# Kernel optimization log

Measured on AMD Instinct MI355X. Metric: run time of the kernel, lower is better.

## Reference

```python
import jax, jax.numpy as jnp
import numpy as np

C_Z = 128
C_HIDDEN = 32
N_HEAD = 4
HC = N_HEAD * C_HIDDEN  # 128
LN_EPS = 1e-5


def setup_inputs() -> dict:
    key = jax.random.key(0)
    ks = jax.random.split(key, 8)
    b, n = 1, 256
    s = 1.0 / np.sqrt(C_Z)
    return {
        "z_ij": jax.random.normal(ks[0], (b, n, n, C_Z), dtype=jnp.float32),
        "ln_gamma": jnp.ones((C_Z,), dtype=jnp.float32),
        "ln_beta": jnp.zeros((C_Z,), dtype=jnp.float32),
        "Wq": jax.random.normal(ks[1], (C_Z, HC), dtype=jnp.float32) * s,
        "Wk": jax.random.normal(ks[2], (C_Z, HC), dtype=jnp.float32) * s,
        "Wv": jax.random.normal(ks[3], (C_Z, HC), dtype=jnp.float32) * s,
        "Wb": jax.random.normal(ks[4], (C_Z, N_HEAD), dtype=jnp.float32) * s,
        "Wg": jax.random.normal(ks[5], (C_Z, HC), dtype=jnp.float32) * s,
        "Wout": jax.random.normal(ks[6], (HC, C_Z), dtype=jnp.float32) * (1.0 / np.sqrt(HC)),
    }


def reference(z_ij, ln_gamma, ln_beta, Wq, Wk, Wv, Wb, Wg, Wout):
    b, n, _, _ = z_ij.shape
    # LayerNorm over c_z
    mu = jnp.mean(z_ij, axis=-1, keepdims=True)
    var = jnp.var(z_ij, axis=-1, keepdims=True)
    z = (z_ij - mu) * jax.lax.rsqrt(var + LN_EPS) * ln_gamma + ln_beta

    def heads(x):  # [b,i,j,hc] -> [b,i,j,h,d]
        return x.reshape(b, n, n, N_HEAD, C_HIDDEN)

    q = heads(z @ Wq)
    k = heads(z @ Wk)
    v = heads(z @ Wv)
    bias = z @ Wb                      # [b,i,j,h]
    g = jax.nn.sigmoid(heads(z @ Wg))  # [b,i,j,h,d]

    scores = jnp.einsum('bijhd,bikhd->bijkh', q, k) / np.sqrt(C_HIDDEN)
    scores = scores + bias[:, None]    # bias[b, j, k, h] broadcast over i
    a = jax.nn.softmax(scores, axis=-2)  # over k
    o = jnp.einsum('bijkh,bikhd->bijhd', a, v)
    o = (g * o).reshape(b, n, n, HC)
    return o @ Wout
```

## Files before the change

### kernel.cpp

```cpp
#include <hip/hip_runtime.h>

typedef _Float16 f16x8 __attribute__((ext_vector_type(8)));
typedef _Float16 f16x2 __attribute__((ext_vector_type(2)));
typedef float f32x4 __attribute__((ext_vector_type(4)));

#define MFMA16(a, b, c) __builtin_amdgcn_mfma_f32_16x16x32_f16(a, b, c, 0, 0, 0)

#define NROW 65536
#define SEGB 16777216ull

__global__ __launch_bounds__(256) void k_ln(
    const float* __restrict__ z, const float* __restrict__ gamma,
    const float* __restrict__ beta, const float* __restrict__ Wb,
    const float* __restrict__ Wq, const float* __restrict__ Wk,
    const float* __restrict__ Wv, const float* __restrict__ Wg,
    const float* __restrict__ Wout,
    _Float16* __restrict__ zln, float* __restrict__ biasT,
    _Float16* __restrict__ WtAll)
{
  __shared__ _Float16 sw[32 * 136];
  int bid = blockIdx.x;
  if (bid < 16384) {
    int lane = threadIdx.x & 63;
    int w = threadIdx.x >> 6;
    int row = bid * 4 + w;
    float2 v = ((const float2*)(z + (size_t)row * 128))[lane];
    float s = v.x + v.y;
    #pragma unroll
    for (int m = 1; m < 64; m <<= 1) s += __shfl_xor(s, m);
    float mu = s * 0.0078125f;
    float dx = v.x - mu, dy = v.y - mu;
    float q = dx * dx + dy * dy;
    #pragma unroll
    for (int m = 1; m < 64; m <<= 1) q += __shfl_xor(q, m);
    float rs = rsqrtf(q * 0.0078125f + 1e-5f);
    float2 g2 = ((const float2*)gamma)[lane];
    float2 b2 = ((const float2*)beta)[lane];
    float y0 = dx * rs * g2.x + b2.x;
    float y1 = dy * rs * g2.y + b2.y;
    f16x2 pr; pr.x = (_Float16)y0; pr.y = (_Float16)y1;
    *(f16x2*)(zln + (size_t)row * 128 + 2 * lane) = pr;
    float4 wb0 = ((const float4*)Wb)[2 * lane];
    float4 wb1 = ((const float4*)Wb)[2 * lane + 1];
    float pb0 = y0 * wb0.x + y1 * wb1.x;
    float pb1 = y0 * wb0.y + y1 * wb1.y;
    float pb2 = y0 * wb0.z + y1 * wb1.z;
    float pb3 = y0 * wb0.w + y1 * wb1.w;
    #pragma unroll
    for (int m = 1; m < 64; m <<= 1) {
      pb0 += __shfl_xor(pb0, m);
      pb1 += __shfl_xor(pb1, m);
      pb2 += __shfl_xor(pb2, m);
      pb3 += __shfl_xor(pb3, m);
    }
    if (lane == 0) {
      biasT[row] = pb0;
      biasT[NROW + row] = pb1;
      biasT[2 * NROW + row] = pb2;
      biasT[3 * NROW + row] = pb3;
    }
  } else {
    int t = bid - 16384;
    int mat = t >> 2, n0 = (t & 3) * 32;
    const float* src = (mat == 0) ? Wq : (mat == 1) ? Wk : (mat == 2) ? Wv
                       : (mat == 3) ? Wg : Wout;
    _Float16* dst = WtAll + mat * 16384;
    for (int it = 0; it < 16; ++it) {
      int e = threadIdx.x + it * 256;
      int c = e >> 5, j = e & 31;
      sw[j * 136 + c] = (_Float16)src[c * 128 + n0 + j];
    }
    __syncthreads();
    for (int it = 0; it < 2; ++it) {
      int ch = threadIdx.x + it * 256;
      int n = ch >> 4, k8 = (ch & 15) * 8;
      *(int4*)(dst + (n0 + n) * 128 + k8) = *(const int4*)&sw[n * 136 + k8];
    }
  }
}

__global__ __launch_bounds__(256) void k_proj(
    const _Float16* __restrict__ A, const _Float16* __restrict__ WtAll,
    _Float16* __restrict__ Qb, _Float16* __restrict__ Kb,
    _Float16* __restrict__ Vb, _Float16* __restrict__ Gb)
{
  __shared__ _Float16 sA[128 * 136];
  __shared__ _Float16 sB[128 * 136];
  int m0 = blockIdx.x * 128;
  int by = blockIdx.y;
  const _Float16* Bt = WtAll + by * 16384;
  _Float16* outp = (by == 0) ? Qb : (by == 1) ? Kb : (by == 2) ? Vb : Gb;
  int tid = threadIdx.x;
  for (int it = 0; it < 8; ++it) {
    int ch = tid + it * 256;
    int r = ch >> 4, c8 = (ch & 15) * 8;
    *(int4*)&sA[r * 136 + c8] = *(const int4*)(A + (size_t)(m0 + r) * 128 + c8);
    *(int4*)&sB[r * 136 + c8] = *(const int4*)(Bt + r * 128 + c8);
  }
  __syncthreads();
  int lane = tid & 63, w = tid >> 6;
  int mw = (w >> 1) * 64, nw = (w & 1) * 64;
  int lr = lane & 15, lg = lane >> 4;
  f32x4 z4 = {0.f, 0.f, 0.f, 0.f};
  f32x4 acc[4][4];
  #pragma unroll
  for (int mt = 0; mt < 4; ++mt)
    #pragma unroll
    for (int nt = 0; nt < 4; ++nt) acc[mt][nt] = z4;
  #pragma unroll
  for (int k0 = 0; k0 < 128; k0 += 32) {
    f16x8 af[4], bf[4];
    #pragma unroll
    for (int mt = 0; mt < 4; ++mt)
      af[mt] = *(const f16x8*)&sA[(mw + mt * 16 + lr) * 136 + k0 + lg * 8];
    #pragma unroll
    for (int nt = 0; nt < 4; ++nt)
      bf[nt] = *(const f16x8*)&sB[(nw + nt * 16 + lr) * 136 + k0 + lg * 8];
    #pragma unroll
    for (int mt = 0; mt < 4; ++mt)
      #pragma unroll
      for (int nt = 0; nt < 4; ++nt)
        acc[mt][nt] = MFMA16(af[mt], bf[nt], acc[mt][nt]);
  }
  bool sig = (by == 3);
  #pragma unroll
  for (int mt = 0; mt < 4; ++mt)
    #pragma unroll
    for (int nt = 0; nt < 4; ++nt)
      #pragma unroll
      for (int r = 0; r < 4; ++r) {
        int row = m0 + mw + mt * 16 + lg * 4 + r;
        int col = nw + nt * 16 + lr;
        float v = acc[mt][nt][r];
        if (sig) v = 1.0f / (1.0f + __expf(-v));
        outp[(size_t)row * 128 + col] = (_Float16)v;
      }
}

__global__ __launch_bounds__(256) void k_attn(
    const _Float16* __restrict__ Qb, const _Float16* __restrict__ Kb,
    const _Float16* __restrict__ Vb, const _Float16* __restrict__ Gb,
    const float* __restrict__ biasT, _Float16* __restrict__ OG)
{
  __shared__ _Float16 sK[256 * 32];
  __shared__ _Float16 sV[32 * 256];
  __shared__ _Float16 sP[64 * 256];
  int i = blockIdx.x, h = blockIdx.y;
  int tid = threadIdx.x;
  size_t base = ((size_t)i * 256) * 128 + h * 32;
  for (int it = 0; it < 4; ++it) {
    int ch = tid + it * 256;
    int r = ch >> 2, cx = ch & 3;
    int p = cx ^ ((r >> 1) & 3);
    *(int4*)&sK[r * 32 + p * 8] = *(const int4*)(Kb + base + (size_t)r * 128 + cx * 8);
  }
  for (int it = 0; it < 4; ++it) {
    int ch = tid + it * 256;
    int k = ch >> 2, d8 = (ch & 3) * 8;
    f16x8 tv = *(const f16x8*)(Vb + base + (size_t)k * 128 + d8);
    #pragma unroll
    for (int jj = 0; jj < 8; ++jj) {
      int d = d8 + jj;
      int p = (k >> 3) ^ (d & 7);
      sV[d * 256 + p * 8 + (k & 7)] = tv[jj];
    }
  }
  __syncthreads();
  int lane = tid & 63, w = tid >> 6;
  int lr = lane & 15, lg = lane >> 4;
  const float scale = 0.17677669529663687f;
  f32x4 z4 = {0.f, 0.f, 0.f, 0.f};
  for (int pass = 0; pass < 4; ++pass) {
    int jbase = pass * 64;
    int jq = jbase + w * 16 + lr;
    f16x8 aq = *(const f16x8*)(Qb + base + (size_t)jq * 128 + lg * 8);
    f32x4 sacc[16];
    #pragma unroll
    for (int kt = 0; kt < 16; ++kt) {
      int r = kt * 16 + lr;
      int p = lg ^ ((r >> 1) & 3);
      f16x8 bk = *(const f16x8*)&sK[r * 32 + p * 8];
      sacc[kt] = MFMA16(aq, bk, z4);
    }
    #pragma unroll
    for (int r = 0; r < 4; ++r) {
      int j = jbase + w * 16 + lg * 4 + r;
      const float* brow = biasT + (size_t)h * NROW + (size_t)j * 256;
      float mx = -1e30f;
      #pragma unroll
      for (int kt = 0; kt < 16; ++kt) {
        float sv = sacc[kt][r] * scale + brow[kt * 16 + lr];
        sacc[kt][r] = sv;
        mx = fmaxf(mx, sv);
      }
      #pragma unroll
      for (int msk = 1; msk < 16; msk <<= 1) mx = fmaxf(mx, __shfl_xor(mx, msk));
      float sum = 0.f;
      #pragma unroll
      for (int kt = 0; kt < 16; ++kt) {
        float pv = __expf(sacc[kt][r] - mx);
        sacc[kt][r] = pv;
        sum += pv;
      }
      #pragma unroll
      for (int msk = 1; msk < 16; msk <<= 1) sum += __shfl_xor(sum, msk);
      float rinv = 1.0f / sum;
      int row = w * 16 + lg * 4 + r;
      #pragma unroll
      for (int kt = 0; kt < 16; ++kt) {
        int k = kt * 16 + lr;
        int pch = (k >> 3) ^ (row & 7);
        sP[row * 256 + pch * 8 + (k & 7)] = (_Float16)(sacc[kt][r] * rinv);
      }
    }
    f32x4 oacc[2] = {z4, z4};
    int prow = w * 16 + lr;
    #pragma unroll
    for (int ks = 0; ks < 8; ++ks) {
      int c = ks * 4 + lg;
      f16x8 ap = *(const f16x8*)&sP[prow * 256 + (c ^ (prow & 7)) * 8];
      #pragma unroll
      for (int nt = 0; nt < 2; ++nt) {
        int d = nt * 16 + lr;
        f16x8 bv = *(const f16x8*)&sV[d * 256 + (c ^ (d & 7)) * 8];
        oacc[nt] = MFMA16(ap, bv, oacc[nt]);
      }
    }
    #pragma unroll
    for (int nt = 0; nt < 2; ++nt)
      #pragma unroll
      for (int r = 0; r < 4; ++r) {
        int j = jbase + w * 16 + lg * 4 + r;
        int d = nt * 16 + lr;
        size_t idx = base + (size_t)j * 128 + d;
        float g = (float)Gb[idx];
        OG[idx] = (_Float16)(oacc[nt][r] * g);
      }
  }
}

__global__ __launch_bounds__(256) void k_outp(
    const _Float16* __restrict__ A, const _Float16* __restrict__ Bt,
    float* __restrict__ out)
{
  __shared__ _Float16 sA[128 * 136];
  __shared__ _Float16 sB[128 * 136];
  int m0 = blockIdx.x * 128;
  int tid = threadIdx.x;
  for (int it = 0; it < 8; ++it) {
    int ch = tid + it * 256;
    int r = ch >> 4, c8 = (ch & 15) * 8;
    *(int4*)&sA[r * 136 + c8] = *(const int4*)(A + (size_t)(m0 + r) * 128 + c8);
    *(int4*)&sB[r * 136 + c8] = *(const int4*)(Bt + r * 128 + c8);
  }
  __syncthreads();
  int lane = tid & 63, w = tid >> 6;
  int mw = (w >> 1) * 64, nw = (w & 1) * 64;
  int lr = lane & 15, lg = lane >> 4;
  f32x4 z4 = {0.f, 0.f, 0.f, 0.f};
  f32x4 acc[4][4];
  #pragma unroll
  for (int mt = 0; mt < 4; ++mt)
    #pragma unroll
    for (int nt = 0; nt < 4; ++nt) acc[mt][nt] = z4;
  #pragma unroll
  for (int k0 = 0; k0 < 128; k0 += 32) {
    f16x8 af[4], bf[4];
    #pragma unroll
    for (int mt = 0; mt < 4; ++mt)
      af[mt] = *(const f16x8*)&sA[(mw + mt * 16 + lr) * 136 + k0 + lg * 8];
    #pragma unroll
    for (int nt = 0; nt < 4; ++nt)
      bf[nt] = *(const f16x8*)&sB[(nw + nt * 16 + lr) * 136 + k0 + lg * 8];
    #pragma unroll
    for (int mt = 0; mt < 4; ++mt)
      #pragma unroll
      for (int nt = 0; nt < 4; ++nt)
        acc[mt][nt] = MFMA16(af[mt], bf[nt], acc[mt][nt]);
  }
  #pragma unroll
  for (int mt = 0; mt < 4; ++mt)
    #pragma unroll
    for (int nt = 0; nt < 4; ++nt)
      #pragma unroll
      for (int r = 0; r < 4; ++r) {
        int row = m0 + mw + mt * 16 + lg * 4 + r;
        int col = nw + nt * 16 + lr;
        out[(size_t)row * 128 + col] = acc[mt][nt][r];
      }
}

extern "C" void kernel_launch(void* const* d_in, const int* in_sizes, int n_in,
                              void* d_out, int out_size, void* d_ws, size_t ws_size,
                              hipStream_t stream) {
  (void)in_sizes; (void)n_in; (void)out_size; (void)ws_size;
  const float* z    = (const float*)d_in[0];
  const float* gam  = (const float*)d_in[1];
  const float* bet  = (const float*)d_in[2];
  const float* Wq   = (const float*)d_in[3];
  const float* Wk   = (const float*)d_in[4];
  const float* Wv   = (const float*)d_in[5];
  const float* Wb   = (const float*)d_in[6];
  const float* Wg   = (const float*)d_in[7];
  const float* Wout = (const float*)d_in[8];

  char* ws = (char*)d_ws;
  _Float16* zln   = (_Float16*)(ws);
  _Float16* Qb    = (_Float16*)(ws + SEGB);
  _Float16* Kb    = (_Float16*)(ws + SEGB * 2);
  _Float16* Vb    = (_Float16*)(ws + SEGB * 3);
  _Float16* Gb    = (_Float16*)(ws + SEGB * 4);
  float*    biasT = (float*)   (ws + SEGB * 5);
  _Float16* WtAll = (_Float16*)(ws + SEGB * 5 + 1048576);

  k_ln<<<16404, 256, 0, stream>>>(z, gam, bet, Wb, Wq, Wk, Wv, Wg, Wout,
                                  zln, biasT, WtAll);
  k_proj<<<dim3(512, 4), 256, 0, stream>>>(zln, WtAll, Qb, Kb, Vb, Gb);
  k_attn<<<dim3(256, 4), 256, 0, stream>>>(Qb, Kb, Vb, Gb, biasT, zln);
  k_outp<<<512, 256, 0, stream>>>(zln, WtAll + 4 * 16384, (float*)d_out);
}
```

Before: 203.2 us.

## Rework pipeline: MFMA bias projection, exp2 softmax without max, gating moved into output GEMM

The LayerNorm kernel now handles two rows per wave with float4 loads and no longer computes the bias. The bias comes from an MFMA projection inside k_proj and is stored in fp16 in a permuted layout that attention can load as vectors. The softmax scale and log2e are folded into Wq and Wb, so attention uses exp2 with a clamp instead of a max-subtract pass. V fragments are kept in registers and the sigmoid gate multiply moves into the output GEMM. The GEMMs drop LDS staging and read fragments straight from global memory. Skipping the max subtraction risks precision loss or overflow for large scores.

Result: slower. 342.2 us (+68.4%).

```diff
diff --git a/kernel.cpp b/kernel.cpp
--- a/kernel.cpp
+++ b/kernel.cpp
@@ -1,149 +1,157 @@
 #include <hip/hip_runtime.h>
 
 typedef _Float16 f16x8 __attribute__((ext_vector_type(8)));
-typedef _Float16 f16x2 __attribute__((ext_vector_type(2)));
+typedef _Float16 f16x4 __attribute__((ext_vector_type(4)));
 typedef float f32x4 __attribute__((ext_vector_type(4)));
 
 #define MFMA16(a, b, c) __builtin_amdgcn_mfma_f32_16x16x32_f16(a, b, c, 0, 0, 0)
-
-#define NROW 65536
 #define SEGB 16777216ull
+
+#define QSCALE ((float)(1.4426950408889634 * 0.17677669529663687))
+#define LOG2E 1.4426950408889634f
 
 __global__ __launch_bounds__(256) void k_ln(
     const float* __restrict__ z, const float* __restrict__ gamma,
-    const float* __restrict__ beta, const float* __restrict__ Wb,
+    const float* __restrict__ beta,
     const float* __restrict__ Wq, const float* __restrict__ Wk,
     const float* __restrict__ Wv, const float* __restrict__ Wg,
-    const float* __restrict__ Wout,
-    _Float16* __restrict__ zln, float* __restrict__ biasT,
-    _Float16* __restrict__ WtAll)
+    const float* __restrict__ Wout, const float* __restrict__ Wb,
+    _Float16* __restrict__ zln, _Float16* __restrict__ WtAll)
 {
   __shared__ _Float16 sw[32 * 136];
   int bid = blockIdx.x;
-  if (bid < 16384) {
+  if (bid < 8192) {
     int lane = threadIdx.x & 63;
     int w = threadIdx.x >> 6;
-    int row = bid * 4 + w;
-    float2 v = ((const float2*)(z + (size_t)row * 128))[lane];
-    float s = v.x + v.y;
-    #pragma unroll
-    for (int m = 1; m < 64; m <<= 1) s += __shfl_xor(s, m);
+    int half = lane >> 5, lh = lane & 31;
+    int row = bid * 8 + w * 2 + half;
+    float4 v = ((const float4*)(z + (size_t)row * 128))[lh];
+    float s = v.x + v.y + v.z + v.w;
+    #pragma unroll
+    for (int m = 1; m < 32; m <<= 1) s += __shfl_xor(s, m);
     float mu = s * 0.0078125f;
-    float dx = v.x - mu, dy = v.y - mu;
-    float q = dx * dx + dy * dy;
-    #pragma unroll
-    for (int m = 1; m < 64; m <<= 1) q += __shfl_xor(q, m);
+    float d0 = v.x - mu, d1 = v.y - mu, d2 = v.z - mu, d3 = v.w - mu;
+    float q = d0 * d0 + d1 * d1 + d2 * d2 + d3 * d3;
+    #pragma unroll
+    for (int m = 1; m < 32; m <<= 1) q += __shfl_xor(q, m);
     float rs = rsqrtf(q * 0.0078125f + 1e-5f);
-    float2 g2 = ((const float2*)gamma)[lane];
-    float2 b2 = ((const float2*)beta)[lane];
-    float y0 = dx * rs * g2.x + b2.x;
-    float y1 = dy * rs * g2.y + b2.y;
-    f16x2 pr; pr.x = (_Float16)y0; pr.y = (_Float16)y1;
-    *(f16x2*)(zln + (size_t)row * 128 + 2 * lane) = pr;
-    float4 wb0 = ((const float4*)Wb)[2 * lane];
-    float4 wb1 = ((const float4*)Wb)[2 * lane + 1];
-    float pb0 = y0 * wb0.x + y1 * wb1.x;
-    float pb1 = y0 * wb0.y + y1 * wb1.y;
-    float pb2 = y0 * wb0.z + y1 * wb1.z;
-    float pb3 = y0 * wb0.w + y1 * wb1.w;
-    #pragma unroll
-    for (int m = 1; m < 64; m <<= 1) {
-      pb0 += __shfl_xor(pb0, m);
-      pb1 += __shfl_xor(pb1, m);
-      pb2 += __shfl_xor(pb2, m);
-      pb3 += __shfl_xor(pb3, m);
-    }
-    if (lane == 0) {
-      biasT[row] = pb0;
-      biasT[NROW + row] = pb1;
-      biasT[2 * NROW + row] = pb2;
-      biasT[3 * NROW + row] = pb3;
-    }
-  } else {
-    int t = bid - 16384;
+    float4 g4 = ((const float4*)gamma)[lh];
+    float4 b4 = ((const float4*)beta)[lh];
+    f16x4 o;
+    o[0] = (_Float16)(d0 * rs * g4.x + b4.x);
+    o[1] = (_Float16)(d1 * rs * g4.y + b4.y);
+    o[2] = (_Float16)(d2 * rs * g4.z + b4.z);
+    o[3] = (_Float16)(d3 * rs * g4.w + b4.w);
+    *(f16x4*)(zln + (size_t)row * 128 + lh * 4) = o;
+  } else if (bid < 8212) {
+    int t = bid - 8192;
     int mat = t >> 2, n0 = (t & 3) * 32;
     const float* src = (mat == 0) ? Wq : (mat == 1) ? Wk : (mat == 2) ? Wv
                        : (mat == 3) ? Wg : Wout;
-    _Float16* dst = WtAll + mat * 16384;
+    float sc = (mat == 0) ? QSCALE : 1.0f;
     for (int it = 0; it < 16; ++it) {
       int e = threadIdx.x + it * 256;
       int c = e >> 5, j = e & 31;
-      sw[j * 136 + c] = (_Float16)src[c * 128 + n0 + j];
+      sw[j * 136 + c] = (_Float16)(src[c * 128 + n0 + j] * sc);
     }
     __syncthreads();
     for (int it = 0; it < 2; ++it) {
       int ch = threadIdx.x + it * 256;
       int n = ch >> 4, k8 = (ch & 15) * 8;
-      *(int4*)(dst + (n0 + n) * 128 + k8) = *(const int4*)&sw[n * 136 + k8];
-    }
-  }
-}
-
-__global__ __launch_bounds__(256) void k_proj(
+      *(int4*)(WtAll + mat * 16384 + (n0 + n) * 128 + k8) =
+          *(const int4*)&sw[n * 136 + k8];
+    }
+  } else {
+    _Float16* WbT = WtAll + 5 * 16384;
+    for (int it = 0; it < 8; ++it) {
+      int e = threadIdx.x + it * 256;
+      if (e < 2048) {
+        int hrow = e >> 7, k = e & 127;
+        float v = (hrow < 4) ? Wb[k * 4 + hrow] * LOG2E : 0.0f;
+        WbT[hrow * 128 + k] = (_Float16)v;
+      }
+    }
+  }
+}
+
+__global__ __launch_bounds__(256, 4) void k_proj(
     const _Float16* __restrict__ A, const _Float16* __restrict__ WtAll,
     _Float16* __restrict__ Qb, _Float16* __restrict__ Kb,
-    _Float16* __restrict__ Vb, _Float16* __restrict__ Gb)
+    _Float16* __restrict__ Vb, _Float16* __restrict__ Gb,
+    _Float16* __restrict__ biasP)
 {
-  __shared__ _Float16 sA[128 * 136];
-  __shared__ _Float16 sB[128 * 136];
   int m0 = blockIdx.x * 128;
   int by = blockIdx.y;
-  const _Float16* Bt = WtAll + by * 16384;
-  _Float16* outp = (by == 0) ? Qb : (by == 1) ? Kb : (by == 2) ? Vb : Gb;
-  int tid = threadIdx.x;
-  for (int it = 0; it < 8; ++it) {
-    int ch = tid + it * 256;
-    int r = ch >> 4, c8 = (ch & 15) * 8;
-    *(int4*)&sA[r * 136 + c8] = *(const int4*)(A + (size_t)(m0 + r) * 128 + c8);
-    *(int4*)&sB[r * 136 + c8] = *(const int4*)(Bt + r * 128 + c8);
-  }
-  __syncthreads();
-  int lane = tid & 63, w = tid >> 6;
-  int mw = (w >> 1) * 64, nw = (w & 1) * 64;
+  int tid = threadIdx.x, lane = tid & 63, w = tid >> 6;
   int lr = lane & 15, lg = lane >> 4;
   f32x4 z4 = {0.f, 0.f, 0.f, 0.f};
-  f32x4 acc[4][4];
-  #pragma unroll
-  for (int mt = 0; mt < 4; ++mt)
-    #pragma unroll
-    for (int nt = 0; nt < 4; ++nt) acc[mt][nt] = z4;
-  #pragma unroll
-  for (int k0 = 0; k0 < 128; k0 += 32) {
-    f16x8 af[4], bf[4];
-    #pragma unroll
-    for (int mt = 0; mt < 4; ++mt)
-      af[mt] = *(const f16x8*)&sA[(mw + mt * 16 + lr) * 136 + k0 + lg * 8];
-    #pragma unroll
-    for (int nt = 0; nt < 4; ++nt)
-      bf[nt] = *(const f16x8*)&sB[(nw + nt * 16 + lr) * 136 + k0 + lg * 8];
-    #pragma unroll
-    for (int mt = 0; mt < 4; ++mt)
-      #pragma unroll
-      for (int nt = 0; nt < 4; ++nt)
-        acc[mt][nt] = MFMA16(af[mt], bf[nt], acc[mt][nt]);
-  }
-  bool sig = (by == 3);
-  #pragma unroll
-  for (int mt = 0; mt < 4; ++mt)
-    #pragma unroll
-    for (int nt = 0; nt < 4; ++nt)
-      #pragma unroll
-      for (int r = 0; r < 4; ++r) {
-        int row = m0 + mw + mt * 16 + lg * 4 + r;
-        int col = nw + nt * 16 + lr;
-        float v = acc[mt][nt][r];
-        if (sig) v = 1.0f / (1.0f + __expf(-v));
-        outp[(size_t)row * 128 + col] = (_Float16)v;
-      }
-}
-
-__global__ __launch_bounds__(256) void k_attn(
+  if (by < 4) {
+    const _Float16* Bt = WtAll + by * 16384;
+    _Float16* outp = (by == 0) ? Qb : (by == 1) ? Kb : (by == 2) ? Vb : Gb;
+    f32x4 acc[2][8];
+    #pragma unroll
+    for (int g = 0; g < 2; ++g)
+      #pragma unroll
+      for (int nt = 0; nt < 8; ++nt) acc[g][nt] = z4;
+    #pragma unroll
+    for (int k0 = 0; k0 < 128; k0 += 32) {
+      f16x8 af[2], bf[8];
+      #pragma unroll
+      for (int g = 0; g < 2; ++g)
+        af[g] = *(const f16x8*)(A + (size_t)(m0 + w * 32 + g * 16 + lr) * 128 + k0 + lg * 8);
+      #pragma unroll
+      for (int nt = 0; nt < 8; ++nt)
+        bf[nt] = *(const f16x8*)(Bt + (nt * 16 + lr) * 128 + k0 + lg * 8);
+      #pragma unroll
+      for (int g = 0; g < 2; ++g)
+        #pragma unroll
+        for (int nt = 0; nt < 8; ++nt)
+          acc[g][nt] = MFMA16(af[g], bf[nt], acc[g][nt]);
+    }
+    bool sig = (by == 3);
+    #pragma unroll
+    for (int g = 0; g < 2; ++g)
+      #pragma unroll
+      for (int nt = 0; nt < 8; ++nt)
+        #pragma unroll
+        for (int r = 0; r < 4; ++r) {
+          int row = m0 + w * 32 + g * 16 + lg * 4 + r;
+          int col = nt * 16 + lr;
+          float v = acc[g][nt][r];
+          if (sig) v = 1.0f / (1.0f + __expf(-v));
+          outp[(size_t)row * 128 + col] = (_Float16)v;
+        }
+  } else {
+    const _Float16* WbT = WtAll + 5 * 16384;
+    f32x4 acc[2] = {z4, z4};
+    #pragma unroll
+    for (int k0 = 0; k0 < 128; k0 += 32) {
+      f16x8 bfb = *(const f16x8*)(WbT + lr * 128 + k0 + lg * 8);
+      #pragma unroll
+      for (int g = 0; g < 2; ++g) {
+        f16x8 afb = *(const f16x8*)(A + (size_t)(m0 + w * 32 + g * 16 + lr) * 128 + k0 + lg * 8);
+        acc[g] = MFMA16(afb, bfb, acc[g]);
+      }
+    }
+    if (lr < 4) {
+      #pragma unroll
+      for (int g = 0; g < 2; ++g)
+        #pragma unroll
+        for (int r = 0; r < 4; ++r) {
+          int R = m0 + w * 32 + g * 16 + lg * 4 + r;
+          biasP[lr * 65536 + (R >> 8) * 256 + (R & 15) * 16 + ((R >> 4) & 15)] =
+              (_Float16)acc[g][r];
+        }
+    }
+  }
+}
+
+__global__ __launch_bounds__(256, 3) void k_attn(
     const _Float16* __restrict__ Qb, const _Float16* __restrict__ Kb,
-    const _Float16* __restrict__ Vb, const _Float16* __restrict__ Gb,
-    const float* __restrict__ biasT, _Float16* __restrict__ OG)
+    const _Float16* __restrict__ Vb, const _Float16* __restrict__ biasP,
+    _Float16* __restrict__ O)
 {
   __shared__ _Float16 sK[256 * 32];
-  __shared__ _Float16 sV[32 * 256];
   __shared__ _Float16 sP[64 * 256];
   int i = blockIdx.x, h = blockIdx.y;
   int tid = threadIdx.x;
@@ -162,14 +170,25 @@
     for (int jj = 0; jj < 8; ++jj) {
       int d = d8 + jj;
       int p = (k >> 3) ^ (d & 7);
-      sV[d * 256 + p * 8 + (k & 7)] = tv[jj];
+      sP[d * 256 + p * 8 + (k & 7)] = tv[jj];
     }
   }
   __syncthreads();
   int lane = tid & 63, w = tid >> 6;
   int lr = lane & 15, lg = lane >> 4;
-  const float scale = 0.17677669529663687f;
+  f16x8 vf[2][8];
+  #pragma unroll
+  for (int ks = 0; ks < 8; ++ks) {
+    int c = ks * 4 + lg;
+    #pragma unroll
+    for (int nt = 0; nt < 2; ++nt) {
+      int d = nt * 16 + lr;
+      vf[nt][ks] = *(const f16x8*)&sP[d * 256 + (c ^ (d & 7)) * 8];
+    }
+  }
+  __syncthreads();
   f32x4 z4 = {0.f, 0.f, 0.f, 0.f};
+  const _Float16* bp = biasP + ((size_t)h << 16);
   for (int pass = 0; pass < 4; ++pass) {
     int jbase = pass * 64;
     int jq = jbase + w * 16 + lr;
@@ -185,25 +204,19 @@
     #pragma unroll
     for (int r = 0; r < 4; ++r) {
       int j = jbase + w * 16 + lg * 4 + r;
-      const float* brow = biasT + (size_t)h * NROW + (size_t)j * 256;
-      float mx = -1e30f;
+      f16x8 b0 = *(const f16x8*)(bp + j * 256 + lr * 16);
+      f16x8 b1 = *(const f16x8*)(bp + j * 256 + lr * 16 + 8);
+      float sum = 0.f;
       #pragma unroll
       for (int kt = 0; kt < 16; ++kt) {
-        float sv = sacc[kt][r] * scale + brow[kt * 16 + lr];
-        sacc[kt][r] = sv;
-        mx = fmaxf(mx, sv);
-      }
-      #pragma unroll
-      for (int msk = 1; msk < 16; msk <<= 1) mx = fmaxf(mx, __shfl_xor(mx, msk));
-      float sum = 0.f;
-      #pragma unroll
-      for (int kt = 0; kt < 16; ++kt) {
-        float pv = __expf(sacc[kt][r] - mx);
-        sacc[kt][r] = pv;
-        sum += pv;
-      }
-      #pragma unroll
-      for (int msk = 1; msk < 16; msk <<= 1) sum += __shfl_xor(sum, msk);
+        float bb = (kt < 8) ? (float)b0[kt] : (float)b1[kt - 8];
+        float sv = fminf(sacc[kt][r] + bb, 80.f);
+        float e = exp2f(sv);
+        sacc[kt][r] = e;
+        sum += e;
+      }
+      #pragma unroll
+      for (int m = 1; m < 16; m <<= 1) sum += __shfl_xor(sum, m);
       float rinv = 1.0f / sum;
       int row = w * 16 + lg * 4 + r;
       #pragma unroll
@@ -220,11 +233,8 @@
       int c = ks * 4 + lg;
       f16x8 ap = *(const f16x8*)&sP[prow * 256 + (c ^ (prow & 7)) * 8];
       #pragma unroll
-      for (int nt = 0; nt < 2; ++nt) {
-        int d = nt * 16 + lr;
-        f16x8 bv = *(const f16x8*)&sV[d * 256 + (c ^ (d & 7)) * 8];
-        oacc[nt] = MFMA16(ap, bv, oacc[nt]);
-      }
+      for (int nt = 0; nt < 2; ++nt)
+        oacc[nt] = MFMA16(ap, vf[nt][ks], oacc[nt]);
     }
     #pragma unroll
     for (int nt = 0; nt < 2; ++nt)
@@ -232,61 +242,52 @@
       for (int r = 0; r < 4; ++r) {
         int j = jbase + w * 16 + lg * 4 + r;
         int d = nt * 16 + lr;
-        size_t idx = base + (size_t)j * 128 + d;
-        float g = (float)Gb[idx];
-        OG[idx] = (_Float16)(oacc[nt][r] * g);
-      }
-  }
-}
-
-__global__ __launch_bounds__(256) void k_outp(
-    const _Float16* __restrict__ A, const _Float16* __restrict__ Bt,
-    float* __restrict__ out)
+        O[base + (size_t)j * 128 + d] = (_Float16)oacc[nt][r];
+      }
+  }
+}
+
+__global__ __launch_bounds__(256, 4) void k_outp(
+    const _Float16* __restrict__ O, const _Float16* __restrict__ G,
+    const _Float16* __restrict__ Bt, float* __restrict__ out)
 {
-  __shared__ _Float16 sA[128 * 136];
-  __shared__ _Float16 sB[128 * 136];
   int m0 = blockIdx.x * 128;
-  int tid = threadIdx.x;
-  for (int it = 0; it < 8; ++it) {
-    int ch = tid + it * 256;
-    int r = ch >> 4, c8 = (ch & 15) * 8;
-    *(int4*)&sA[r * 136 + c8] = *(const int4*)(A + (size_t)(m0 + r) * 128 + c8);
-    *(int4*)&sB[r * 136 + c8] = *(const int4*)(Bt + r * 128 + c8);
-  }
-  __syncthreads();
-  int lane = tid & 63, w = tid >> 6;
-  int mw = (w >> 1) * 64, nw = (w & 1) * 64;
+  int tid = threadIdx.x, lane = tid & 63, w = tid >> 6;
   int lr = lane & 15, lg = lane >> 4;
   f32x4 z4 = {0.f, 0.f, 0.f, 0.f};
-  f32x4 acc[4][4];
+  f32x4 acc[2][8];
   #pragma unroll
-  for (int mt = 0; mt < 4; ++mt)
-    #pragma unroll
-    for (int nt = 0; nt < 4; ++nt) acc[mt][nt] = z4;
+  for (int g = 0; g < 2; ++g)
+    #pragma unroll
+    for (int nt = 0; nt < 8; ++nt) acc[g][nt] = z4;
   #pragma unroll
   for (int k0 = 0; k0 < 128; k0 += 32) {
-    f16x8 af[4], bf[4];
-    #pragma unroll
-    for (int mt = 0; mt < 4; ++mt)
-      af[mt] = *(const f16x8*)&sA[(mw + mt * 16 + lr) * 136 + k0 + lg * 8];
-    #pragma unroll
-    for (int nt = 0; nt < 4; ++nt)
-      bf[nt] = *(const f16x8*)&sB[(nw + nt * 16 + lr) * 136 + k0 + lg * 8];
-    #pragma unroll
-    for (int mt = 0; mt < 4; ++mt)
-      #pragma unroll
-      for (int nt = 0; nt < 4; ++nt)
-        acc[mt][nt] = MFMA16(af[mt], bf[nt], acc[mt][nt]);
+    f16x8 af[2], bf[8];
+    #pragma unroll
+    for (int g = 0; g < 2; ++g) {
+      size_t a = (size_t)(m0 + w * 32 + g * 16 + lr) * 128 + k0 + lg * 8;
+      f16x8 o8 = *(const f16x8*)(O + a);
+      f16x8 g8 = *(const f16x8*)(G + a);
+      af[g] = o8 * g8;
+    }
+    #pragma unroll
+    for (int nt = 0; nt < 8; ++nt)
+      bf[nt] = *(const f16x8*)(Bt + (nt * 16 + lr) * 128 + k0 + lg * 8);
+    #pragma unroll
+    for (int g = 0; g < 2; ++g)
+      #pragma unroll
+      for (int nt = 0; nt < 8; ++nt)
+        acc[g][nt] = MFMA16(af[g], bf[nt], acc[g][nt]);
   }
   #pragma unroll
-  for (int mt = 0; mt < 4; ++mt)
-    #pragma unroll
-    for (int nt = 0; nt < 4; ++nt)
+  for (int g = 0; g < 2; ++g)
+    #pragma unroll
+    for (int nt = 0; nt < 8; ++nt)
       #pragma unroll
       for (int r = 0; r < 4; ++r) {
-        int row = m0 + mw + mt * 16 + lg * 4 + r;
-        int col = nw + nt * 16 + lr;
-        out[(size_t)row * 128 + col] = acc[mt][nt][r];
+        int row = m0 + w * 32 + g * 16 + lg * 4 + r;
+        int col = nt * 16 + lr;
+        out[(size_t)row * 128 + col] = acc[g][nt][r];
       }
 }
 
@@ -310,12 +311,12 @@
   _Float16* Kb    = (_Float16*)(ws + SEGB * 2);
   _Float16* Vb    = (_Float16*)(ws + SEGB * 3);
   _Float16* Gb    = (_Float16*)(ws + SEGB * 4);
-  float*    biasT = (float*)   (ws + SEGB * 5);
+  _Float16* biasP = (_Float16*)(ws + SEGB * 5);
   _Float16* WtAll = (_Float16*)(ws + SEGB * 5 + 1048576);
 
-  k_ln<<<16404, 256, 0, stream>>>(z, gam, bet, Wb, Wq, Wk, Wv, Wg, Wout,
-                                  zln, biasT, WtAll);
-  k_proj<<<dim3(512, 4), 256, 0, stream>>>(zln, WtAll, Qb, Kb, Vb, Gb);
-  k_attn<<<dim3(256, 4), 256, 0, stream>>>(Qb, Kb, Vb, Gb, biasT, zln);
-  k_outp<<<512, 256, 0, stream>>>(zln, WtAll + 4 * 16384, (float*)d_out);
-}
+  k_ln<<<8213, 256, 0, stream>>>(z, gam, bet, Wq, Wk, Wv, Wg, Wout, Wb,
+                                 zln, WtAll);
+  k_proj<<<dim3(512, 5), 256, 0, stream>>>(zln, WtAll, Qb, Kb, Vb, Gb, biasP);
+  k_attn<<<dim3(256, 4), 256, 0, stream>>>(Qb, Kb, Vb, biasP, zln);
+  k_outp<<<512, 256, 0, stream>>>(zln, Gb, WtAll + 4 * 16384, (float*)d_out);
+}
```
